# Kernel optimization log

Hardware: AMD Instinct MI355X
Metric: run time of the kernel (lower is better)

The kernel has to match this reference:

```python
import jax, jax.numpy as jnp
import numpy as np

B, S, D = 4, 1024, 512      # batch, seq_len, input_dim (== layer_size)
M = 64                      # meta_memory_dim
L = 2                       # n_hidden_layers in ResLinear memory MLP
H = 8                       # num_attention_heads
WIN = 128                   # attention_window_size (causal sliding window)
LR, WD, MAX_ALR = 1e-3, 1e-2, 0.1
EPS = 1e-8                  # AdamW eps (betas 0.9/0.999; first step => m_hat=g, v_hat=g^2)


def lmm_fwd(lmm_W, lmm_b, x):
    # ResLinear: residual MLP, h <- h + silu(h @ W_i + b_i)
    h = x
    for i in range(L):
        h = h + jax.nn.silu(h @ lmm_W[i] + lmm_b[i])
    return h


def sliding_window_attn(x, swa_W, swa_b):
    Bsz, T, _ = x.shape
    hd = D // H
    q = (x @ swa_W[0] + swa_b[0]).reshape(Bsz, T, H, hd)
    k = (x @ swa_W[1] + swa_b[1]).reshape(Bsz, T, H, hd)
    v = (x @ swa_W[2] + swa_b[2]).reshape(Bsz, T, H, hd)
    scores = jnp.einsum('bihd,bjhd->bhij', q, k) / np.float32(np.sqrt(hd))
    i = jnp.arange(T)[:, None]
    j = jnp.arange(T)[None, :]
    mask = (j <= i) & (j > i - WIN)
    scores = jnp.where(mask, scores, jnp.float32(-1e30))
    attn = jax.nn.softmax(scores, axis=-1)
    o = jnp.einsum('bhij,bjhd->bihd', attn, v).reshape(Bsz, T, D)
    return o @ swa_W[3] + swa_b[3]


def setup_inputs() -> dict:
    key = jax.random.key(0)
    ks = jax.random.split(key, 9)
    sc = np.float32(1.0 / np.sqrt(D))
    s = lambda k, shape: jax.random.normal(k, shape, jnp.float32) * sc
    return {
        'x': jax.random.normal(ks[0], (B, S, D), jnp.float32),
        'meta_memory': jax.random.normal(ks[1], (M, D), jnp.float32),
        'lmm_W': s(ks[2], (L, D, D)),
        'lmm_b': jnp.zeros((L, D), jnp.float32),
        'Wq': s(ks[3], (D, D)), 'bq': jnp.zeros((D,), jnp.float32),
        'Wk': s(ks[4], (D, D)), 'bk': jnp.zeros((D,), jnp.float32),
        'Wv': s(ks[5], (D, D)), 'bv': jnp.zeros((D,), jnp.float32),
        'W_lr': s(ks[6], (D, 1)), 'b_lr': jnp.zeros((1,), jnp.float32),
        'swa_W': s(ks[7], (4, D, D)),  # q,k,v,out projections of SWA
        'swa_b': jnp.zeros((4, D), jnp.float32),
    }


def reference(x, meta_memory, lmm_W, lmm_b, Wq, bq, Wk, bk, Wv, bv, W_lr, b_lr, swa_W, swa_b):
    Bsz = x.shape[0]
    # inject meta memory tokens
    meta = jnp.broadcast_to(meta_memory, (Bsz, M, D))
    xm = jnp.concatenate([meta, x], axis=1)            # [B, M+S, D]

    q = xm @ Wq + bq                                   # queries  [B, T, D]
    k = xm @ Wk + bk                                   # keys
    v = xm @ Wv + bv                                   # values
    w = (jax.nn.sigmoid(xm @ W_lr + b_lr) * MAX_ALR)[..., 0]  # adaptive lr [B, T]

    # inner-loop meta-gradient of the weighted associative loss w.r.t. memory params
    def assoc_loss(params):
        preds = lmm_fwd(params[0], params[1], k)
        loss = jnp.mean((preds - v) ** 2, axis=-1)     # [B, T]
        return jnp.sum(loss * w)

    gW, gb = jax.grad(assoc_loss)((lmm_W, lmm_b))

    # one AdamW step from freshly-initialized optimizer state:
    # m_hat = g, v_hat = g^2  =>  p' = p*(1 - lr*wd) - lr * g / (|g| + eps)
    adamw = lambda p, g: p * (1.0 - LR * WD) - LR * g / (jnp.abs(g) + EPS)
    W1, b1 = adamw(lmm_W, gW), adamw(lmm_b, gb)

    # retrieval with updated memory + sliding-window attention
    retrieved = lmm_fwd(W1, b1, q)                     # [B, T, D]
    out = sliding_window_attn(retrieved, swa_W, swa_b)
    return out[:, M:, :]                               # discard meta tokens -> [B, S, D]
```

## Files before the change

kernel.cpp:

```cpp
#include <hip/hip_runtime.h>
#include <cmath>

constexpr int BB = 4, SSQ = 1024, DD = 512, MM = 64, TTK = MM + SSQ;
constexpr int HH = 8, HD = DD / HH, WINDOW = 128;
constexpr int RROWS = BB * TTK;
constexpr int OROWS = BB * SSQ;
constexpr float LR_ = 1e-3f, WD_ = 1e-2f, MAXALR_ = 0.1f, EPS_ = 1e-8f;
constexpr float C2_ = 2.0f / (float)DD;
constexpr int VPAD = 200;
constexpr int SPLITK = 17;

typedef short  s16x8 __attribute__((ext_vector_type(8)));
typedef float  f32x4 __attribute__((ext_vector_type(4)));

__device__ __forceinline__ float b2f(unsigned short u) {
    union { unsigned int i; float f; } c; c.i = ((unsigned int)u) << 16; return c.f;
}
__device__ __forceinline__ unsigned short f2b(float f) {
    union { float f; unsigned int i; } c; c.f = f;
    unsigned int r = c.i + 0x7fffu + ((c.i >> 16) & 1u);
    return (unsigned short)(r >> 16);
}
__device__ __forceinline__ float sigm(float x) { return 1.f / (1.f + __expf(-x)); }

__device__ __forceinline__ void gld16(const void* g, void* l) {
    __builtin_amdgcn_global_load_lds((const __attribute__((address_space(1))) unsigned int*)g,
                                     (__attribute__((address_space(3))) unsigned int*)l, 16, 0, 0);
}

template<int EPI, int TNN, bool WTR, bool GBS>
__global__ __launch_bounds__(512) void mgemm(
    const unsigned short* __restrict__ A, const unsigned short* __restrict__ Bm,
    const float* __restrict__ bias,
    const unsigned short* __restrict__ aux0, const unsigned short* __restrict__ aux1,
    const float* __restrict__ wrow,
    void* __restrict__ out0, unsigned short* __restrict__ out1,
    unsigned short* __restrict__ outT, int tc0, int tc1, float* __restrict__ gbOut,
    int M, int N, int K, int lda, int ld0, int ld1)
{
    constexpr int WCOLS = TNN / 4;
    constexpr int NJ = WCOLS / 16;
    constexpr int NB = TNN / 64;
    constexpr int ASZ = 128 * 64;
    constexpr int BSZ = TNN * 64;
    __shared__ __align__(16) unsigned short LB[2 * ASZ + 2 * BSZ];
    __shared__ float gacc[128];

    const int tid = threadIdx.x;
    const int m0 = blockIdx.y * 128, n0 = blockIdx.x * TNN;
    const int ktiles = K >> 6;
    const int per = ktiles / gridDim.z;
    const int kt0 = blockIdx.z * per, kt1 = kt0 + per;

    if (GBS && tid < 128) gacc[tid] = 0.f;

    const int r_ = tid >> 3, c_ = tid & 7;

    auto stage = [&](int buf, int kt) {
        const size_t kb = (size_t)kt * 64;
        const int sw = (c_ ^ (r_ & 7)) * 8;
#pragma unroll
        for (int p = 0; p < 2; ++p) {
            int row = p * 64 + r_;
            gld16(A + (size_t)(m0 + row) * lda + kb + sw,
                  &LB[buf * ASZ + row * 64 + c_ * 8]);
        }
#pragma unroll
        for (int p = 0; p < NB; ++p) {
            int row = p * 64 + r_;
            gld16(Bm + (size_t)(n0 + row) * K + kb + sw,
                  &LB[2 * ASZ + buf * BSZ + row * 64 + c_ * 8]);
        }
    };

    f32x4 acc[4][NJ];
#pragma unroll
    for (int i = 0; i < 4; ++i)
#pragma unroll
        for (int j = 0; j < NJ; ++j)
#pragma unroll
            for (int r = 0; r < 4; ++r) acc[i][j][r] = 0.f;

    const int lane = tid & 63, wv = tid >> 6;
    const int wr = wv & 1, wc = wv >> 1;
    const int fr = lane & 15, fg = lane >> 4;

    stage(0, kt0);
    int cur = 0;
    for (int kt = kt0; kt < kt1; ++kt) {
        __syncthreads();
        if (kt + 1 < kt1) stage(cur ^ 1, kt + 1);
#pragma unroll
        for (int ks = 0; ks < 2; ++ks) {
            s16x8 a[4], b[NJ];
#pragma unroll
            for (int i = 0; i < 4; ++i) {
                const int arow = wr * 64 + i * 16 + fr;
                a[i] = *(const s16x8*)&LB[cur * ASZ + arow * 64 + (((ks * 4 + fg) ^ (arow & 7)) * 8)];
            }
#pragma unroll
            for (int j = 0; j < NJ; ++j) {
                const int brow = wc * WCOLS + j * 16 + fr;
                b[j] = *(const s16x8*)&LB[2 * ASZ + cur * BSZ + brow * 64 + (((ks * 4 + fg) ^ (brow & 7)) * 8)];
            }
#pragma unroll
            for (int i = 0; i < 4; ++i)
#pragma unroll
                for (int j = 0; j < NJ; ++j)
                    acc[i][j] = __builtin_amdgcn_mfma_f32_16x16x32_bf16(a[i], b[j], acc[i][j], 0, 0, 0);
        }
        cur ^= 1;
    }
    __syncthreads();

    const bool wtr_blk = WTR && (n0 >= tc0) && (n0 < tc1);
    unsigned short* TL = LB;

    float gsum[NJ];
#pragma unroll
    for (int j = 0; j < NJ; ++j) gsum[j] = 0.f;

#pragma unroll
    for (int j = 0; j < NJ; ++j) {
        const int col = n0 + wc * WCOLS + j * 16 + fr;
        const float bj = (EPI == 6 || bias == nullptr) ? 0.f : bias[col];
#pragma unroll
        for (int i = 0; i < 4; ++i) {
            const int rowb = m0 + wr * 64 + i * 16 + fg * 4;
#pragma unroll
            for (int r = 0; r < 4; ++r) {
                const int row = rowb + r;
                const size_t off  = (size_t)row * N + col;
                const size_t off0 = (size_t)row * ld0 + col;
                const size_t off1 = (size_t)row * ld1 + col;
                float val = acc[i][j][r] + bj;
                float tv = val;
                if constexpr (EPI == 0) {
                    ((unsigned short*)out0)[off] = f2b(val);
                } else if constexpr (EPI == 1 || EPI == 2) {
                    float base = b2f(aux0[off0]);
                    float h = base + val * sigm(val);
                    ((unsigned short*)out0)[off] = f2b(h);
                    if constexpr (EPI == 2) out1[off] = f2b(val);
                    tv = h;
                } else if constexpr (EPI == 3) {
                    float h1 = b2f(aux0[off0]);
                    float pred = h1 + val * sigm(val);
                    float vv = b2f(aux1[off1]);
                    float d2 = C2_ * wrow[row] * (pred - vv);
                    float s = sigm(val);
                    float dz2 = d2 * (s * (1.f + val * (1.f - s)));
                    ((unsigned short*)out0)[off] = f2b(d2);
                    out1[off] = f2b(dz2);
                    tv = dz2;
                } else if constexpr (EPI == 4) {
                    float dh = val + b2f(aux0[off0]);
                    float z1 = b2f(aux1[off1]);
                    float s = sigm(z1);
                    float dz1v = dh * (s * (1.f + z1 * (1.f - s)));
                    ((unsigned short*)out0)[off] = f2b(dz1v);
                    tv = dz1v;
                } else if constexpr (EPI == 5) {
                    ((float*)out0)[off] = val;
                } else {
                    ((float*)out0)[(size_t)blockIdx.z * ld0 + off] = val;
                }
                if (wtr_blk)
                    TL[(size_t)(col - n0) * 136 + (row - m0)] = f2b(tv);
                if constexpr (GBS) gsum[j] += tv;
            }
        }
    }

    if constexpr (GBS) {
#pragma unroll
        for (int j = 0; j < NJ; ++j) {
            float s = gsum[j];
            s += __shfl_xor(s, 16);
            s += __shfl_xor(s, 32);
            if (lane < 16) atomicAdd(&gacc[wc * WCOLS + j * 16 + fr], s);
        }
    }

    if (wtr_blk || GBS) {
        __syncthreads();
        if (wtr_blk) {
            for (int idx = tid; idx < TNN * 16; idx += 512) {
                int c = idx >> 4, ch = idx & 15;
                s16x8 v = *(const s16x8*)&TL[(size_t)c * 136 + ch * 8];
                *(s16x8*)&outT[(size_t)(n0 - tc0 + c) * M + m0 + ch * 8] = v;
            }
        }
        if (GBS && tid < TNN) atomicAdd(gbOut + n0 + tid, gacc[tid]);
    }
}

struct TXP { const float* s[10]; unsigned short* d[10]; };
__global__ __launch_bounds__(256) void mega_setup(TXP p,
    const float* __restrict__ x, const float* __restrict__ meta, unsigned short* __restrict__ xm,
    const float* __restrict__ Wlr, const float* __restrict__ blr, float* __restrict__ w,
    const float* bq, const float* bk, const float* bv,
    const float* sb, float* cb1, float* cb2, float* gb)
{
    const int bid = blockIdx.x, tid = threadIdx.x;
    if (bid < 640) {
        __shared__ unsigned short t[64][65];
        int z = bid >> 6;
        const float* src = p.s[z];
        unsigned short* dst = p.d[z];
        int r0 = ((bid >> 3) & 7) * 64, c0 = (bid & 7) * 64;
        int lr = tid >> 4, lc = (tid & 15) * 4;
        if (z == 9) {
#pragma unroll
            for (int rr = 0; rr < 64; rr += 16) {
                size_t base = (size_t)(r0 + lr + rr) * 512 + c0 + lc;
                float4 v = *(const float4*)(src + base);
                ushort4 o; o.x = f2b(v.x); o.y = f2b(v.y); o.z = f2b(v.z); o.w = f2b(v.w);
                *(ushort4*)(dst + base) = o;
            }
            return;
        }
#pragma unroll
        for (int rr = 0; rr < 64; rr += 16) {
            float4 v = *(const float4*)(src + (size_t)(r0 + lr + rr) * 512 + c0 + lc);
            t[lr + rr][lc] = f2b(v.x); t[lr + rr][lc + 1] = f2b(v.y);
            t[lr + rr][lc + 2] = f2b(v.z); t[lr + rr][lc + 3] = f2b(v.w);
        }
        __syncthreads();
#pragma unroll
        for (int cc = 0; cc < 64; cc += 16) {
            int c = lr + cc;
            ushort4 o; o.x = t[lc][c]; o.y = t[lc + 1][c]; o.z = t[lc + 2][c]; o.w = t[lc + 3][c];
            *(ushort4*)(dst + (size_t)(c0 + c) * 512 + r0 + lc) = o;
        }
        return;
    }
    if (bid < 640 + RROWS) {
        __shared__ float sm[4];
        int row = bid - 640;
        int b = row / TTK, tt = row % TTK;
        const float* src = (tt < MM) ? meta + (size_t)tt * DD
                                     : x + ((size_t)b * SSQ + (tt - MM)) * DD;
        float x0 = src[tid], x1 = src[tid + 256];
        unsigned short* dst = xm + (size_t)row * DD;
        dst[tid] = f2b(x0); dst[tid + 256] = f2b(x1);
        float s = x0 * Wlr[tid] + x1 * Wlr[tid + 256];
        for (int o2 = 32; o2; o2 >>= 1) s += __shfl_down(s, o2);
        if ((tid & 63) == 0) sm[tid >> 6] = s;
        __syncthreads();
        if (tid == 0) w[row] = MAXALR_ / (1.f + __expf(-(sm[0] + sm[1] + sm[2] + sm[3] + blr[0])));
        return;
    }
    int i = (bid - 640 - RROWS) * 256 + tid;
    if (i < 1536) {
        float v = (i < 512) ? bq[i] : (i < 1024) ? bk[i - 512] : bv[i - 1024];
        cb1[i] = v; cb2[i] = sb[i];
    } else if (i < 2560) {
        gb[i - 1536] = 0.f;
    }
}

__global__ __launch_bounds__(256) void adamw_transp(const float* __restrict__ W,
                                                    const float* __restrict__ gWp,
                                                    unsigned short* __restrict__ dstBase,
                                                    const float* __restrict__ pb,
                                                    const float* __restrict__ gB,
                                                    float* __restrict__ bnOut) {
    if (blockIdx.z == 2) {
        int idx = (blockIdx.y * 8 + blockIdx.x) * 256 + threadIdx.x;
        if (idx < 2 * DD) {
            float gg = gB[idx];
            bnOut[idx] = pb[idx] * (1.f - LR_ * WD_) - LR_ * gg / (fabsf(gg) + EPS_);
        }
        return;
    }
    const int m = blockIdx.z;
    const float* src = W + (size_t)m * DD * DD;
    unsigned short* dst = dstBase + (size_t)m * DD * DD;
    __shared__ unsigned short t[64][65];
    int r0 = blockIdx.y * 64, c0 = blockIdx.x * 64;
    int lr = threadIdx.x >> 4, lc = (threadIdx.x & 15) * 4;
#pragma unroll
    for (int rr = 0; rr < 64; rr += 16) {
        size_t base = (size_t)(r0 + lr + rr) * 512 + c0 + lc;
        float4 v = *(const float4*)(src + base);
        float gx = 0.f, gy = 0.f, gz = 0.f, gw = 0.f;
        for (int z = 0; z < SPLITK; ++z) {
            const float4 p4 = *(const float4*)(gWp + ((size_t)z * 2 + m) * DD * DD + base);
            gx += p4.x; gy += p4.y; gz += p4.z; gw += p4.w;
        }
        t[lr + rr][lc]     = f2b(v.x * (1.f - LR_ * WD_) - LR_ * gx / (fabsf(gx) + EPS_));
        t[lr + rr][lc + 1] = f2b(v.y * (1.f - LR_ * WD_) - LR_ * gy / (fabsf(gy) + EPS_));
        t[lr + rr][lc + 2] = f2b(v.z * (1.f - LR_ * WD_) - LR_ * gz / (fabsf(gz) + EPS_));
        t[lr + rr][lc + 3] = f2b(v.w * (1.f - LR_ * WD_) - LR_ * gw / (fabsf(gw) + EPS_));
    }
    __syncthreads();
#pragma unroll
    for (int cc = 0; cc < 64; cc += 16) {
        int c = lr + cc;
        ushort4 o; o.x = t[lc][c]; o.y = t[lc + 1][c]; o.z = t[lc + 2][c]; o.w = t[lc + 3][c];
        *(ushort4*)(dst + (size_t)(c0 + c) * 512 + r0 + lc) = o;
    }
}

__global__ __launch_bounds__(256) void swa_mfma(const unsigned short* __restrict__ AQ,
                                                unsigned short* __restrict__ O) {
    __shared__ unsigned short Qs[64 * 64];
    __shared__ unsigned short KP[192 * 64];
    __shared__ unsigned short Vt[64 * VPAD];

    const int tid = threadIdx.x;
    const int qt = blockIdx.x, h = blockIdx.y, b = blockIdx.z;
    const int i0 = MM + qt * 64;
    const int jbase = i0 - 128;
    const int r_ = tid >> 3, c_ = tid & 7;

#pragma unroll
    for (int rd = 0; rd < 2; ++rd) {
        int r = rd * 32 + r_;
        const unsigned short* src = AQ + ((size_t)(b * TTK + i0 + r)) * 1536 + h * HD
                                    + ((c_ ^ (r & 7)) * 8);
        gld16(src, &Qs[rd * 2048 + tid * 8]);
    }
#pragma unroll
    for (int rd = 0; rd < 6; ++rd) {
        int r = rd * 32 + r_;
        int j = jbase + r; if (j < 0) j = 0;
        const unsigned short* src = AQ + ((size_t)(b * TTK + j)) * 1536 + 512 + h * HD
                                    + ((c_ ^ (r & 7)) * 8);
        gld16(src, &KP[rd * 2048 + tid * 8]);
    }
#pragma unroll
    for (int rd = 0; rd < 6; ++rd) {
        int r = rd * 32 + r_;
        int j = jbase + r; if (j < 0) j = 0;
        const s16x8 vv = *(const s16x8*)(AQ + ((size_t)(b * TTK + j)) * 1536 + 1024 + h * HD + c_ * 8);
#pragma unroll
        for (int i = 0; i < 8; ++i)
            Vt[(c_ * 8 + i) * VPAD + r] = (unsigned short)vv[i];
    }
    __syncthreads();

    const int lane = tid & 63, w = tid >> 6;
    const int g = lane >> 4, fl = lane & 15;
    const int qA = w * 16 + fl;
    const int swzA = qA & 7;

    f32x4 sc[12];
#pragma unroll
    for (int t = 0; t < 12; ++t) { sc[t][0] = 0.f; sc[t][1] = 0.f; sc[t][2] = 0.f; sc[t][3] = 0.f; }

#pragma unroll
    for (int ks = 0; ks < 2; ++ks) {
        s16x8 af = *(const s16x8*)&Qs[qA * 64 + (((4 * ks + g) ^ swzA) * 8)];
#pragma unroll
        for (int t = 0; t < 12; ++t) {
            int jn = t * 16 + fl;
            s16x8 bf = *(const s16x8*)&KP[jn * 64 + (((4 * ks + g) ^ (jn & 7)) * 8)];
            sc[t] = __builtin_amdgcn_mfma_f32_16x16x32_bf16(af, bf, sc[t], 0, 0, 0);
        }
    }

    const int kmin = (i0 < 128) ? (128 - i0) : 0;
    float mx[4] = {-1e30f, -1e30f, -1e30f, -1e30f};
#pragma unroll
    for (int t = 0; t < 12; ++t) {
        int kk = t * 16 + fl;
#pragma unroll
        for (int r = 0; r < 4; ++r) {
            int qb = w * 16 + g * 4 + r;
            bool m = (kk > qb) && (kk <= qb + 128) && (kk >= kmin);
            float v = m ? sc[t][r] * 0.125f : -1e30f;
            sc[t][r] = v;
            mx[r] = fmaxf(mx[r], v);
        }
    }
#pragma unroll
    for (int r = 0; r < 4; ++r) {
        mx[r] = fmaxf(mx[r], __shfl_xor(mx[r], 1));
        mx[r] = fmaxf(mx[r], __shfl_xor(mx[r], 2));
        mx[r] = fmaxf(mx[r], __shfl_xor(mx[r], 4));
        mx[r] = fmaxf(mx[r], __shfl_xor(mx[r], 8));
    }
    float ls[4] = {0.f, 0.f, 0.f, 0.f};
#pragma unroll
    for (int t = 0; t < 12; ++t) {
#pragma unroll
        for (int r = 0; r < 4; ++r) {
            float p = __expf(sc[t][r] - mx[r]);
            sc[t][r] = p;
            ls[r] += p;
        }
    }
#pragma unroll
    for (int r = 0; r < 4; ++r) {
        ls[r] += __shfl_xor(ls[r], 1);
        ls[r] += __shfl_xor(ls[r], 2);
        ls[r] += __shfl_xor(ls[r], 4);
        ls[r] += __shfl_xor(ls[r], 8);
    }

    __syncthreads();

#pragma unroll
    for (int t = 0; t < 12; ++t) {
        int kk = t * 16 + fl;
#pragma unroll
        for (int r = 0; r < 4; ++r) {
            int qb = w * 16 + g * 4 + r;
            int ch = (kk >> 3) ^ (qb & 7);
            KP[qb * 192 + ch * 8 + (kk & 7)] = f2b(sc[t][r]);
        }
    }
    __syncthreads();

    f32x4 oacc[4];
#pragma unroll
    for (int dt = 0; dt < 4; ++dt) { oacc[dt][0] = 0.f; oacc[dt][1] = 0.f; oacc[dt][2] = 0.f; oacc[dt][3] = 0.f; }
#pragma unroll
    for (int js = 0; js < 6; ++js) {
        s16x8 pa = *(const s16x8*)&KP[qA * 192 + (((js * 4 + g) ^ swzA) * 8)];
#pragma unroll
        for (int dt = 0; dt < 4; ++dt) {
            s16x8 bv = *(const s16x8*)&Vt[(dt * 16 + fl) * VPAD + js * 32 + g * 8];
            oacc[dt] = __builtin_amdgcn_mfma_f32_16x16x32_bf16(pa, bv, oacc[dt], 0, 0, 0);
        }
    }

    float inv[4];
#pragma unroll
    for (int r = 0; r < 4; ++r) inv[r] = 1.f / ls[r];
#pragma unroll
    for (int dt = 0; dt < 4; ++dt) {
#pragma unroll
        for (int r = 0; r < 4; ++r) {
            int qb = w * 16 + g * 4 + r;
            int srow = qt * 64 + qb;
            int d = dt * 16 + fl;
            O[((size_t)b * SSQ + srow) * DD + h * HD + d] = f2b(oacc[dt][r] * inv[r]);
        }
    }
}

extern "C" void kernel_launch(void* const* d_in, const int* in_sizes, int n_in,
                              void* d_out, int out_size, void* d_ws, size_t ws_size,
                              hipStream_t stream) {
    const float* x    = (const float*)d_in[0];
    const float* meta = (const float*)d_in[1];
    const float* lmmW = (const float*)d_in[2];
    const float* lmmb = (const float*)d_in[3];
    const float* Wq   = (const float*)d_in[4];
    const float* bq   = (const float*)d_in[5];
    const float* Wk   = (const float*)d_in[6];
    const float* bk   = (const float*)d_in[7];
    const float* Wv   = (const float*)d_in[8];
    const float* bv   = (const float*)d_in[9];
    const float* Wlr  = (const float*)d_in[10];
    const float* blr  = (const float*)d_in[11];
    const float* swaW = (const float*)d_in[12];
    const float* swab = (const float*)d_in[13];
    float* out = (float*)d_out;
    (void)in_sizes; (void)n_in; (void)out_size; (void)ws_size;

    char* wsb = (char*)d_ws;
    size_t off = 0;
    auto alloc = [&](size_t bytes) -> void* {
        void* p = wsb + off; off = (off + bytes + 255) & ~(size_t)255; return p;
    };
    const size_t BIGE = (size_t)RROWS * DD;
    unsigned short* qkv  = (unsigned short*)alloc((size_t)RROWS * 1536 * 2);
    unsigned short* xm   = (unsigned short*)alloc(BIGE * 2);
    unsigned short* h1   = (unsigned short*)alloc(BIGE * 2);
    unsigned short* z1   = (unsigned short*)alloc(BIGE * 2);
    unsigned short* d2   = (unsigned short*)alloc(BIGE * 2);
    unsigned short* dz2  = (unsigned short*)alloc(BIGE * 2);
    unsigned short* dz1  = (unsigned short*)alloc(BIGE * 2);
    unsigned short* h1r  = (unsigned short*)alloc(BIGE * 2);
    unsigned short* retr = (unsigned short*)alloc(BIGE * 2);
    unsigned short* o    = (unsigned short*)alloc((size_t)OROWS * DD * 2);
    unsigned short* kT   = (unsigned short*)alloc(BIGE * 2);
    unsigned short* h1T  = (unsigned short*)alloc(BIGE * 2);
    unsigned short* dz2T = (unsigned short*)alloc(BIGE * 2);
    unsigned short* dz1T = (unsigned short*)alloc(BIGE * 2);
    unsigned short* Wt   = (unsigned short*)alloc((size_t)12 * DD * DD * 2);
    float* gWp  = (float*)alloc((size_t)SPLITK * 2 * DD * DD * 4);
    float* w    = (float*)alloc((size_t)RROWS * 4);
    float* gb   = (float*)alloc(1024 * 4);
    float* bn   = (float*)alloc(1024 * 4);
    float* cbQ  = (float*)alloc(1536 * 4);
    float* cbS  = (float*)alloc(1536 * 4);
    auto WT = [&](int i) { return Wt + (size_t)i * DD * DD; };

    TXP tp{};
    tp.s[0] = Wq;             tp.d[0] = WT(0);
    tp.s[1] = Wk;             tp.d[1] = WT(1);
    tp.s[2] = Wv;             tp.d[2] = WT(2);
    tp.s[3] = lmmW;           tp.d[3] = WT(3);
    tp.s[4] = lmmW + DD * DD; tp.d[4] = WT(4);
    tp.s[5] = swaW + 0 * DD * DD; tp.d[5] = WT(5);
    tp.s[6] = swaW + 1 * DD * DD; tp.d[6] = WT(6);
    tp.s[7] = swaW + 2 * DD * DD; tp.d[7] = WT(7);
    tp.s[8] = swaW + 3 * DD * DD; tp.d[8] = WT(8);
    tp.s[9] = lmmW + DD * DD; tp.d[9] = WT(9);
    mega_setup<<<640 + RROWS + 10, 256, 0, stream>>>(tp, x, meta, xm, Wlr, blr, w,
                                                     bq, bk, bv, swab, cbQ, cbS, gb);

    const dim3 gB(512);
    const dim3 gF(12, 34, 1);
    const dim3 g64(8, 34, 1);
    const dim3 gTN(4, 4, SPLITK);
    const dim3 gO64(8, 32, 1);

    mgemm<0, 128, true, false><<<gF, gB, 0, stream>>>(xm, WT(0), cbQ, nullptr, nullptr, nullptr,
                                                      qkv, nullptr, kT, 512, 1024, nullptr,
                                                      RROWS, 1536, DD, DD, 0, 0);

    mgemm<2, 64, true, false><<<g64, gB, 0, stream>>>(qkv + 512, WT(3), lmmb, qkv + 512, nullptr, nullptr,
                                                      h1, z1, h1T, 0, 512, nullptr,
                                                      RROWS, DD, DD, 1536, 1536, 0);
    mgemm<3, 64, true, true><<<g64, gB, 0, stream>>>(h1, WT(4), lmmb + DD, h1, qkv + 1024, w,
                                                     d2, dz2, dz2T, 0, 512, gb + DD,
                                                     RROWS, DD, DD, DD, DD, 1536);

    mgemm<6, 128, false, false><<<gTN, gB, 0, stream>>>(h1T, dz2T, nullptr, nullptr, nullptr, nullptr,
                                                        gWp + DD * DD, nullptr, nullptr, 0, 0, nullptr,
                                                        DD, DD, RROWS, RROWS, 2 * DD * DD, 0);
    mgemm<4, 64, true, true><<<g64, gB, 0, stream>>>(dz2, WT(9), nullptr, d2, z1, nullptr,
                                                     dz1, nullptr, dz1T, 0, 512, gb,
                                                     RROWS, DD, DD, DD, DD, DD);
    mgemm<6, 128, false, false><<<gTN, gB, 0, stream>>>(kT, dz1T, nullptr, nullptr, nullptr, nullptr,
                                                        gWp, nullptr, nullptr, 0, 0, nullptr,
                                                        DD, DD, RROWS, RROWS, 2 * DD * DD, 0);

    adamw_transp<<<dim3(8, 8, 3), 256, 0, stream>>>(lmmW, gWp, WT(10), lmmb, gb, bn);

    mgemm<1, 64, false, false><<<g64, gB, 0, stream>>>(qkv, WT(10), bn, qkv, nullptr, nullptr,
                                                       h1r, nullptr, nullptr, 0, 0, nullptr,
                                                       RROWS, DD, DD, 1536, 1536, 0);
    mgemm<1, 64, false, false><<<g64, gB, 0, stream>>>(h1r, WT(11), bn + DD, h1r, nullptr, nullptr,
                                                       retr, nullptr, nullptr, 0, 0, nullptr,
                                                       RROWS, DD, DD, DD, DD, 0);

    mgemm<0, 128, false, false><<<gF, gB, 0, stream>>>(retr, WT(5), cbS, nullptr, nullptr, nullptr,
                                                       qkv, nullptr, nullptr, 0, 0, nullptr,
                                                       RROWS, 1536, DD, DD, 0, 0);
    swa_mfma<<<dim3(16, 8, 4), 256, 0, stream>>>(qkv, o);
    mgemm<5, 64, false, false><<<gO64, gB, 0, stream>>>(o, WT(8), swab + 3 * DD, nullptr, nullptr, nullptr,
                                                        out, nullptr, nullptr, 0, 0, nullptr,
                                                        OROWS, DD, DD, DD, 0, 0);
}
```

Before: 236.7 us.

## Halve GEMM M-tile to 64 rows and fuse independent weight-grad and dz1 GEMMs

Adds a TMM template parameter and switches every GEMM from 128-row to 64-row tiles, doubling block counts to fill more compute units on this small problem. It also merges the split-K h1T×dz2T weight-gradient GEMM with the independent dz1 backward GEMM into one launch that dispatches on block index, so the two run concurrently and one launch is saved. The cost is less data reuse per block (more B-tile reloads), and the transpose write path now depends on the tile-size constants and hard-coded block-count splits.

```diff
diff --git a/kernel.cpp b/kernel.cpp
--- a/kernel.cpp
+++ b/kernel.cpp
@@ -28,29 +28,34 @@
                                      (__attribute__((address_space(3))) unsigned int*)l, 16, 0, 0);
 }
 
-template<int EPI, int TNN, bool WTR, bool GBS>
-__global__ __launch_bounds__(512) void mgemm(
-    const unsigned short* __restrict__ A, const unsigned short* __restrict__ Bm,
-    const float* __restrict__ bias,
-    const unsigned short* __restrict__ aux0, const unsigned short* __restrict__ aux1,
-    const float* __restrict__ wrow,
-    void* __restrict__ out0, unsigned short* __restrict__ out1,
-    unsigned short* __restrict__ outT, int tc0, int tc1, float* __restrict__ gbOut,
-    int M, int N, int K, int lda, int ld0, int ld1)
+struct GArgs {
+    const unsigned short* A; const unsigned short* Bm;
+    const float* bias;
+    const unsigned short* aux0; const unsigned short* aux1;
+    const float* wrow;
+    void* out0; unsigned short* out1;
+    unsigned short* outT; int tc0, tc1; float* gbOut;
+    int M, N, K, lda, ld0, ld1;
+};
+
+template<int EPI, int TMM, int TNN, bool WTR, bool GBS>
+__device__ __forceinline__ void mgemm_body(unsigned short* __restrict__ LB, float* __restrict__ gacc,
+                                           int bx, int by, int bz, int gz, const GArgs& a, int tid)
 {
     constexpr int WCOLS = TNN / 4;
     constexpr int NJ = WCOLS / 16;
-    constexpr int NB = TNN / 64;
-    constexpr int ASZ = 128 * 64;
+    constexpr int NI = TMM / 32;
+    constexpr int APASS = TMM / 64;
+    constexpr int BPASS = TNN / 64;
+    constexpr int ASZ = TMM * 64;
     constexpr int BSZ = TNN * 64;
-    __shared__ __align__(16) unsigned short LB[2 * ASZ + 2 * BSZ];
-    __shared__ float gacc[128];
-
-    const int tid = threadIdx.x;
-    const int m0 = blockIdx.y * 128, n0 = blockIdx.x * TNN;
-    const int ktiles = K >> 6;
-    const int per = ktiles / gridDim.z;
-    const int kt0 = blockIdx.z * per, kt1 = kt0 + per;
+    constexpr int TP  = TMM + 8;
+    constexpr int CH  = TMM / 8;
+
+    const int m0 = by * TMM, n0 = bx * TNN;
+    const int ktiles = a.K >> 6;
+    const int per = ktiles / gz;
+    const int kt0 = bz * per, kt1 = kt0 + per;
 
     if (GBS && tid < 128) gacc[tid] = 0.f;
 
@@ -60,22 +65,22 @@
         const size_t kb = (size_t)kt * 64;
         const int sw = (c_ ^ (r_ & 7)) * 8;
 #pragma unroll
-        for (int p = 0; p < 2; ++p) {
+        for (int p = 0; p < APASS; ++p) {
             int row = p * 64 + r_;
-            gld16(A + (size_t)(m0 + row) * lda + kb + sw,
+            gld16(a.A + (size_t)(m0 + row) * a.lda + kb + sw,
                   &LB[buf * ASZ + row * 64 + c_ * 8]);
         }
 #pragma unroll
-        for (int p = 0; p < NB; ++p) {
+        for (int p = 0; p < BPASS; ++p) {
             int row = p * 64 + r_;
-            gld16(Bm + (size_t)(n0 + row) * K + kb + sw,
+            gld16(a.Bm + (size_t)(n0 + row) * a.K + kb + sw,
                   &LB[2 * ASZ + buf * BSZ + row * 64 + c_ * 8]);
         }
     };
 
-    f32x4 acc[4][NJ];
-#pragma unroll
-    for (int i = 0; i < 4; ++i)
+    f32x4 acc[NI][NJ];
+#pragma unroll
+    for (int i = 0; i < NI; ++i)
 #pragma unroll
         for (int j = 0; j < NJ; ++j)
 #pragma unroll
@@ -92,28 +97,28 @@
         if (kt + 1 < kt1) stage(cur ^ 1, kt + 1);
 #pragma unroll
         for (int ks = 0; ks < 2; ++ks) {
-            s16x8 a[4], b[NJ];
-#pragma unroll
-            for (int i = 0; i < 4; ++i) {
-                const int arow = wr * 64 + i * 16 + fr;
-                a[i] = *(const s16x8*)&LB[cur * ASZ + arow * 64 + (((ks * 4 + fg) ^ (arow & 7)) * 8)];
+            s16x8 av[NI], bv[NJ];
+#pragma unroll
+            for (int i = 0; i < NI; ++i) {
+                const int arow = wr * (TMM / 2) + i * 16 + fr;
+                av[i] = *(const s16x8*)&LB[cur * ASZ + arow * 64 + (((ks * 4 + fg) ^ (arow & 7)) * 8)];
             }
 #pragma unroll
             for (int j = 0; j < NJ; ++j) {
                 const int brow = wc * WCOLS + j * 16 + fr;
-                b[j] = *(const s16x8*)&LB[2 * ASZ + cur * BSZ + brow * 64 + (((ks * 4 + fg) ^ (brow & 7)) * 8)];
+                bv[j] = *(const s16x8*)&LB[2 * ASZ + cur * BSZ + brow * 64 + (((ks * 4 + fg) ^ (brow & 7)) * 8)];
             }
 #pragma unroll
-            for (int i = 0; i < 4; ++i)
+            for (int i = 0; i < NI; ++i)
 #pragma unroll
                 for (int j = 0; j < NJ; ++j)
-                    acc[i][j] = __builtin_amdgcn_mfma_f32_16x16x32_bf16(a[i], b[j], acc[i][j], 0, 0, 0);
+                    acc[i][j] = __builtin_amdgcn_mfma_f32_16x16x32_bf16(av[i], bv[j], acc[i][j], 0, 0, 0);
         }
         cur ^= 1;
     }
     __syncthreads();
 
-    const bool wtr_blk = WTR && (n0 >= tc0) && (n0 < tc1);
+    const bool wtr_blk = WTR && (n0 >= a.tc0) && (n0 < a.tc1);
     unsigned short* TL = LB;
 
     float gsum[NJ];
@@ -123,50 +128,50 @@
 #pragma unroll
     for (int j = 0; j < NJ; ++j) {
         const int col = n0 + wc * WCOLS + j * 16 + fr;
-        const float bj = (EPI == 6 || bias == nullptr) ? 0.f : bias[col];
-#pragma unroll
-        for (int i = 0; i < 4; ++i) {
-            const int rowb = m0 + wr * 64 + i * 16 + fg * 4;
+        const float bj = (EPI == 6 || a.bias == nullptr) ? 0.f : a.bias[col];
+#pragma unroll
+        for (int i = 0; i < NI; ++i) {
+            const int rowb = m0 + wr * (TMM / 2) + i * 16 + fg * 4;
 #pragma unroll
             for (int r = 0; r < 4; ++r) {
                 const int row = rowb + r;
-                const size_t off  = (size_t)row * N + col;
-                const size_t off0 = (size_t)row * ld0 + col;
-                const size_t off1 = (size_t)row * ld1 + col;
+                const size_t off  = (size_t)row * a.N + col;
+                const size_t off0 = (size_t)row * a.ld0 + col;
+                const size_t off1 = (size_t)row * a.ld1 + col;
                 float val = acc[i][j][r] + bj;
                 float tv = val;
                 if constexpr (EPI == 0) {
-                    ((unsigned short*)out0)[off] = f2b(val);
+                    ((unsigned short*)a.out0)[off] = f2b(val);
                 } else if constexpr (EPI == 1 || EPI == 2) {
-                    float base = b2f(aux0[off0]);
+                    float base = b2f(a.aux0[off0]);
                     float h = base + val * sigm(val);
-                    ((unsigned short*)out0)[off] = f2b(h);
-                    if constexpr (EPI == 2) out1[off] = f2b(val);
+                    ((unsigned short*)a.out0)[off] = f2b(h);
+                    if constexpr (EPI == 2) a.out1[off] = f2b(val);
                     tv = h;
                 } else if constexpr (EPI == 3) {
-                    float h1 = b2f(aux0[off0]);
+                    float h1 = b2f(a.aux0[off0]);
                     float pred = h1 + val * sigm(val);
-                    float vv = b2f(aux1[off1]);
-                    float d2 = C2_ * wrow[row] * (pred - vv);
+                    float vv = b2f(a.aux1[off1]);
+                    float d2 = C2_ * a.wrow[row] * (pred - vv);
                     float s = sigm(val);
                     float dz2 = d2 * (s * (1.f + val * (1.f - s)));
-                    ((unsigned short*)out0)[off] = f2b(d2);
-                    out1[off] = f2b(dz2);
+                    ((unsigned short*)a.out0)[off] = f2b(d2);
+                    a.out1[off] = f2b(dz2);
                     tv = dz2;
                 } else if constexpr (EPI == 4) {
-                    float dh = val + b2f(aux0[off0]);
-                    float z1 = b2f(aux1[off1]);
+                    float dh = val + b2f(a.aux0[off0]);
+                    float z1 = b2f(a.aux1[off1]);
                     float s = sigm(z1);
                     float dz1v = dh * (s * (1.f + z1 * (1.f - s)));
-                    ((unsigned short*)out0)[off] = f2b(dz1v);
+                    ((unsigned short*)a.out0)[off] = f2b(dz1v);
                     tv = dz1v;
                 } else if constexpr (EPI == 5) {
-                    ((float*)out0)[off] = val;
+                    ((float*)a.out0)[off] = val;
                 } else {
-                    ((float*)out0)[(size_t)blockIdx.z * ld0 + off] = val;
+                    ((float*)a.out0)[(size_t)bz * a.ld0 + off] = val;
                 }
                 if (wtr_blk)
-                    TL[(size_t)(col - n0) * 136 + (row - m0)] = f2b(tv);
+                    TL[(size_t)(col - n0) * TP + (row - m0)] = f2b(tv);
                 if constexpr (GBS) gsum[j] += tv;
             }
         }
@@ -185,13 +190,34 @@
     if (wtr_blk || GBS) {
         __syncthreads();
         if (wtr_blk) {
-            for (int idx = tid; idx < TNN * 16; idx += 512) {
-                int c = idx >> 4, ch = idx & 15;
-                s16x8 v = *(const s16x8*)&TL[(size_t)c * 136 + ch * 8];
-                *(s16x8*)&outT[(size_t)(n0 - tc0 + c) * M + m0 + ch * 8] = v;
+            for (int idx = tid; idx < TNN * CH; idx += 512) {
+                int c = idx / CH, ch = idx % CH;
+                s16x8 v = *(const s16x8*)&TL[(size_t)c * TP + ch * 8];
+                *(s16x8*)&a.outT[(size_t)(n0 - a.tc0 + c) * a.M + m0 + ch * 8] = v;
             }
         }
-        if (GBS && tid < TNN) atomicAdd(gbOut + n0 + tid, gacc[tid]);
+        if (GBS && tid < TNN) atomicAdd(a.gbOut + n0 + tid, gacc[tid]);
+    }
+}
+
+template<int EPI, int TMM, int TNN, bool WTR, bool GBS>
+__global__ __launch_bounds__(512) void mgemm(GArgs a) {
+    __shared__ __align__(16) unsigned short LB[2 * TMM * 64 + 2 * TNN * 64];
+    __shared__ float gacc[128];
+    mgemm_body<EPI, TMM, TNN, WTR, GBS>(LB, gacc, blockIdx.x, blockIdx.y, blockIdx.z,
+                                        gridDim.z, a, threadIdx.x);
+}
+
+__global__ __launch_bounds__(512) void mgemm_dual(GArgs a1, GArgs a2) {
+    __shared__ __align__(16) unsigned short LB[2 * 64 * 64 + 2 * 128 * 64];
+    __shared__ float gacc[128];
+    int bid = blockIdx.x;
+    if (bid < 544) {
+        int bz = bid >> 5, rem = bid & 31;
+        mgemm_body<6, 64, 128, false, false>(LB, gacc, rem & 3, rem >> 2, bz, SPLITK, a1, threadIdx.x);
+    } else {
+        bid -= 544;
+        mgemm_body<4, 64, 64, true, true>(LB, gacc, bid & 7, bid >> 3, 0, 1, a2, threadIdx.x);
     }
 }
 
@@ -505,47 +531,50 @@
     mega_setup<<<640 + RROWS + 10, 256, 0, stream>>>(tp, x, meta, xm, Wlr, blr, w,
                                                      bq, bk, bv, swab, cbQ, cbS, gb);
 
+    auto ga = [](const unsigned short* A, const unsigned short* Bm, const float* bias,
+                 const unsigned short* a0, const unsigned short* a1, const float* wr,
+                 void* o0, unsigned short* o1, unsigned short* oT, int t0, int t1, float* gbo,
+                 int M, int N, int K, int lda, int l0, int l1) {
+        GArgs g{A, Bm, bias, a0, a1, wr, o0, o1, oT, t0, t1, gbo, M, N, K, lda, l0, l1};
+        return g;
+    };
     const dim3 gB(512);
-    const dim3 gF(12, 34, 1);
-    const dim3 g64(8, 34, 1);
-    const dim3 gTN(4, 4, SPLITK);
-    const dim3 gO64(8, 32, 1);
-
-    mgemm<0, 128, true, false><<<gF, gB, 0, stream>>>(xm, WT(0), cbQ, nullptr, nullptr, nullptr,
-                                                      qkv, nullptr, kT, 512, 1024, nullptr,
-                                                      RROWS, 1536, DD, DD, 0, 0);
-
-    mgemm<2, 64, true, false><<<g64, gB, 0, stream>>>(qkv + 512, WT(3), lmmb, qkv + 512, nullptr, nullptr,
-                                                      h1, z1, h1T, 0, 512, nullptr,
-                                                      RROWS, DD, DD, 1536, 1536, 0);
-    mgemm<3, 64, true, true><<<g64, gB, 0, stream>>>(h1, WT(4), lmmb + DD, h1, qkv + 1024, w,
-                                                     d2, dz2, dz2T, 0, 512, gb + DD,
-                                                     RROWS, DD, DD, DD, DD, 1536);
-
-    mgemm<6, 128, false, false><<<gTN, gB, 0, stream>>>(h1T, dz2T, nullptr, nullptr, nullptr, nullptr,
-                                                        gWp + DD * DD, nullptr, nullptr, 0, 0, nullptr,
-                                                        DD, DD, RROWS, RROWS, 2 * DD * DD, 0);
-    mgemm<4, 64, true, true><<<g64, gB, 0, stream>>>(dz2, WT(9), nullptr, d2, z1, nullptr,
-                                                     dz1, nullptr, dz1T, 0, 512, gb,
-                                                     RROWS, DD, DD, DD, DD, DD);
-    mgemm<6, 128, false, false><<<gTN, gB, 0, stream>>>(kT, dz1T, nullptr, nullptr, nullptr, nullptr,
-                                                        gWp, nullptr, nullptr, 0, 0, nullptr,
-                                                        DD, DD, RROWS, RROWS, 2 * DD * DD, 0);
+
+    mgemm<0, 64, 128, true, false><<<dim3(12, 68), gB, 0, stream>>>(
+        ga(xm, WT(0), cbQ, nullptr, nullptr, nullptr, qkv, nullptr, kT, 512, 1024, nullptr,
+           RROWS, 1536, DD, DD, 0, 0));
+
+    mgemm<2, 64, 64, true, false><<<dim3(8, 68), gB, 0, stream>>>(
+        ga(qkv + 512, WT(3), lmmb, qkv + 512, nullptr, nullptr, h1, z1, h1T, 0, 512, nullptr,
+           RROWS, DD, DD, 1536, 1536, 0));
+    mgemm<3, 64, 64, true, true><<<dim3(8, 68), gB, 0, stream>>>(
+        ga(h1, WT(4), lmmb + DD, h1, qkv + 1024, w, d2, dz2, dz2T, 0, 512, gb + DD,
+           RROWS, DD, DD, DD, DD, 1536));
+
+    mgemm_dual<<<1088, gB, 0, stream>>>(
+        ga(h1T, dz2T, nullptr, nullptr, nullptr, nullptr, gWp + DD * DD, nullptr, nullptr, 0, 0, nullptr,
+           DD, DD, RROWS, RROWS, 2 * DD * DD, 0),
+        ga(dz2, WT(9), nullptr, d2, z1, nullptr, dz1, nullptr, dz1T, 0, 512, gb,
+           RROWS, DD, DD, DD, DD, DD));
+
+    mgemm<6, 64, 128, false, false><<<dim3(4, 8, SPLITK), gB, 0, stream>>>(
+        ga(kT, dz1T, nullptr, nullptr, nullptr, nullptr, gWp, nullptr, nullptr, 0, 0, nullptr,
+           DD, DD, RROWS, RROWS, 2 * DD * DD, 0));
 
     adamw_transp<<<dim3(8, 8, 3), 256, 0, stream>>>(lmmW, gWp, WT(10), lmmb, gb, bn);
 
-    mgemm<1, 64, false, false><<<g64, gB, 0, stream>>>(qkv, WT(10), bn, qkv, nullptr, nullptr,
-                                                       h1r, nullptr, nullptr, 0, 0, nullptr,
-                                                       RROWS, DD, DD, 1536, 1536, 0);
-    mgemm<1, 64, false, false><<<g64, gB, 0, stream>>>(h1r, WT(11), bn + DD, h1r, nullptr, nullptr,
-                                                       retr, nullptr, nullptr, 0, 0, nullptr,
-                                                       RROWS, DD, DD, DD, DD, 0);
-
-    mgemm<0, 128, false, false><<<gF, gB, 0, stream>>>(retr, WT(5), cbS, nullptr, nullptr, nullptr,
-                                                       qkv, nullptr, nullptr, 0, 0, nullptr,
-                                                       RROWS, 1536, DD, DD, 0, 0);
+    mgemm<1, 64, 64, false, false><<<dim3(8, 68), gB, 0, stream>>>(
+        ga(qkv, WT(10), bn, qkv, nullptr, nullptr, h1r, nullptr, nullptr, 0, 0, nullptr,
+           RROWS, DD, DD, 1536, 1536, 0));
+    mgemm<1, 64, 64, false, false><<<dim3(8, 68), gB, 0, stream>>>(
+        ga(h1r, WT(11), bn + DD, h1r, nullptr, nullptr, retr, nullptr, nullptr, 0, 0, nullptr,
+           RROWS, DD, DD, DD, DD, 0));
+
+    mgemm<0, 64, 128, false, false><<<dim3(12, 68), gB, 0, stream>>>(
+        ga(retr, WT(5), cbS, nullptr, nullptr, nullptr, qkv, nullptr, nullptr, 0, 0, nullptr,
+           RROWS, 1536, DD, DD, 0, 0));
     swa_mfma<<<dim3(16, 8, 4), 256, 0, stream>>>(qkv, o);
-    mgemm<5, 64, false, false><<<gO64, gB, 0, stream>>>(o, WT(8), swab + 3 * DD, nullptr, nullptr, nullptr,
-                                                        out, nullptr, nullptr, 0, 0, nullptr,
-                                                        OROWS, DD, DD, DD, 0, 0);
-}
+    mgemm<5, 64, 64, false, false><<<dim3(8, 64), gB, 0, stream>>>(
+        ga(o, WT(8), swab + 3 * DD, nullptr, nullptr, nullptr, out, nullptr, nullptr, 0, 0, nullptr,
+           OROWS, DD, DD, DD, 0, 0));
+}
```

New measurement: 224.9 us. 1.05x faster.
